# Kernel optimization log

Measured on AMD Instinct MI355X. Metric: run time of the kernel, lower is better.

Reference implementation:

```python
import jax, jax.numpy as jnp
import numpy as np

NUM_HEADS = 8
DIM_HEAD = 64
GROUPS = 32
EPS = 1e-5


def setup_inputs() -> dict:
    key = jax.random.key(0)
    k1, k2, k3 = jax.random.split(key, 3)
    C = 512
    inner = NUM_HEADS * DIM_HEAD  # 512
    x = jax.random.normal(k1, (8, C, 32, 32), dtype=jnp.float32)
    gamma = jnp.ones((C,), dtype=jnp.float32)
    beta = jnp.zeros((C,), dtype=jnp.float32)
    w_qkv = jax.random.normal(k2, (3 * inner, C), dtype=jnp.float32) * 0.02
    w_out = jax.random.normal(k3, (C, inner), dtype=jnp.float32) * 0.02
    return {"x": x, "gamma": gamma, "beta": beta, "w_qkv": w_qkv, "w_out": w_out}


def group_norm(x, gamma, beta):
    b, c, h, w = x.shape
    xg = x.reshape(b, GROUPS, c // GROUPS, h, w)
    mean = jnp.mean(xg, axis=(2, 3, 4), keepdims=True)
    var = jnp.var(xg, axis=(2, 3, 4), keepdims=True)
    xn = ((xg - mean) * jax.lax.rsqrt(var + EPS)).reshape(b, c, h, w)
    return xn * gamma[None, :, None, None] + beta[None, :, None, None]


def reference(x, gamma, beta, w_qkv, w_out):
    b, c, h, w = x.shape
    H, d = NUM_HEADS, DIM_HEAD
    inner = H * d
    scale = d ** (-0.5)
    residual = x
    xn = group_norm(x, gamma, beta)
    # 1x1 conv (no bias) == channel matmul
    qkv = jnp.einsum('bchw,oc->bohw', xn, w_qkv)  # [b, 3*inner, h, w]
    q, k, v = jnp.split(qkv, 3, axis=1)
    def to_heads(t):
        # b (H d) h w -> b H (h w) d
        return t.reshape(b, H, d, h * w).transpose(0, 1, 3, 2)
    q, k, v = to_heads(q), to_heads(k), to_heads(v)
    attn = jnp.einsum('bhid,bhjd->bhij', q, k) * scale  # [b,H,hw,hw]
    attn = jax.nn.softmax(attn, axis=-1)
    out = jnp.einsum('bhij,bhjd->bhid', attn, v)  # [b,H,hw,d]
    # b H (h w) d -> b (H d) h w
    out = out.transpose(0, 1, 3, 2).reshape(b, inner, h, w)
    out = jnp.einsum('bchw,oc->bohw', out, w_out)
    return out + residual
```

## Files before the change

### kernel.cpp

```cpp
#include <hip/hip_runtime.h>


typedef __attribute__((ext_vector_type(8))) short bf16x8;
typedef __attribute__((ext_vector_type(4))) float f32x4;

#define NB 8
#define NC 512
#define HW 1024
#define NHEAD 8
#define DHEAD 64
#define GROUPS 32
#define CPG 16
#define QKV_N 1536

#define GLL16(gaddr, ldsaddr)                                                  \
    __builtin_amdgcn_global_load_lds(                                          \
        (const __attribute__((address_space(1))) unsigned*)(gaddr),            \
        (__attribute__((address_space(3))) unsigned*)(ldsaddr), 16, 0, 0)

__device__ alignas(64) short g_xn[(size_t)8192 * 512];
__device__ alignas(64) short g_qkv[(size_t)8192 * 1536];
__device__ alignas(64) short g_vt[(size_t)64 * 64 * 1024];
__device__ alignas(64) short g_attno[(size_t)8192 * 512];
__device__ alignas(64) short g_wqkv[(size_t)1536 * 512];
__device__ alignas(64) short g_wout[(size_t)512 * 512];

__device__ __forceinline__ float b2f(short h) {
    union { unsigned u; float f; } v;
    v.u = ((unsigned)(unsigned short)h) << 16;
    return v.f;
}
__device__ __forceinline__ short f2b(float f) {
    union { float f; unsigned u; } v;
    v.f = f;
    unsigned r = v.u + 0x7fff + ((v.u >> 16) & 1);
    return (short)(r >> 16);
}

__global__ __launch_bounds__(256) void conv_weights(
    const float* __restrict__ wqkv, const float* __restrict__ wout) {
    int i = blockIdx.x * 256 + threadIdx.x;
    if (i < 1536 * 512) {
        float v = wqkv[i];
        if (i < 512 * 512) v *= 0.125f;
        g_wqkv[i] = f2b(v);
    }
    if (i < 512 * 512)  g_wout[i] = f2b(wout[i]);
}

__global__ __launch_bounds__(256) void gn_kernel(
    const float* __restrict__ x, const float* __restrict__ gamma,
    const float* __restrict__ beta) {
    int b = blockIdx.x >> 5, g = blockIdx.x & 31;
    int tid = threadIdx.x;
    __shared__ alignas(16) short tile[CPG][HW];
    __shared__ float red[2][4];
    __shared__ float sg[CPG], sb[CPG];
    if (tid < CPG) {
        int cg = g * CPG + tid;
        sg[tid] = gamma[cg];
        sb[tid] = beta[cg];
    }
    const float* xb = x + (size_t)b * NC * HW + (size_t)g * CPG * HW;
    float s1 = 0.f, s2 = 0.f;
    #pragma unroll
    for (int it = 0; it < 8; it++) {
        int idx = tid + it * 256;
        f32x4 v0 = *(const f32x4*)(xb + idx * 8);
        f32x4 v1 = *(const f32x4*)(xb + idx * 8 + 4);
        bf16x8 w;
        #pragma unroll
        for (int j = 0; j < 4; j++) {
            s1 += v0[j] + v1[j]; s2 += v0[j] * v0[j] + v1[j] * v1[j];
            w[j] = f2b(v0[j]); w[j + 4] = f2b(v1[j]);
        }
        *(bf16x8*)(&((short*)tile)[idx * 8]) = w;
    }
    #pragma unroll
    for (int off = 32; off; off >>= 1) { s1 += __shfl_xor(s1, off); s2 += __shfl_xor(s2, off); }
    int wid = tid >> 6;
    if ((tid & 63) == 0) { red[0][wid] = s1; red[1][wid] = s2; }
    __syncthreads();
    float t1 = red[0][0] + red[0][1] + red[0][2] + red[0][3];
    float t2 = red[1][0] + red[1][1] + red[1][2] + red[1][3];
    float mean = t1 * (1.f / 16384.f);
    float var  = t2 * (1.f / 16384.f) - mean * mean;
    float inv  = rsqrtf(var + 1e-5f);
    #pragma unroll
    for (int p = 0; p < 4; p++) {
        int s = tid * 4 + p;
        bf16x8 pk0, pk1;
        #pragma unroll
        for (int cc = 0; cc < 8; cc++) {
            pk0[cc] = f2b((b2f(tile[cc][s])     - mean) * inv * sg[cc]     + sb[cc]);
            pk1[cc] = f2b((b2f(tile[cc + 8][s]) - mean) * inv * sg[cc + 8] + sb[cc + 8]);
        }
        size_t dst = ((size_t)(b * HW + s)) * NC + g * CPG;
        *(bf16x8*)(g_xn + dst)     = pk0;
        *(bf16x8*)(g_xn + dst + 8) = pk1;
    }
}

__global__ __launch_bounds__(256) void gemm_qkv() {
    const int K = NC;
    int tid = threadIdx.x, lane = tid & 63, wid = tid >> 6;
    int quad = lane >> 4, l15 = lane & 15;
    int row0 = blockIdx.x * 128;
    int col0 = blockIdx.y * 128;
    __shared__ alignas(16) short sa[128 * 32];
    __shared__ alignas(16) short sbuf[128 * 32];
    int srow = wid * 32 + (lane >> 2);
    int scol = (lane & 3) * 8;
    const short* ga = g_xn   + (size_t)(row0 + srow) * K + scol;
    const short* gb = g_wqkv + (size_t)(col0 + srow) * K + scol;
    short* la = sa   + wid * 1024;
    short* lb = sbuf + wid * 1024;
    int mw = (wid >> 1) * 64, nw = (wid & 1) * 64;
    f32x4 acc[4][4] = {};
    for (int k = 0; k < K; k += 32) {
        GLL16(ga + k, la);
        GLL16(ga + (size_t)16 * K + k, la + 512);
        GLL16(gb + k, lb);
        GLL16(gb + (size_t)16 * K + k, lb + 512);
        __syncthreads();
        bf16x8 af[4], bfv[4];
        #pragma unroll
        for (int m = 0; m < 4; m++) af[m]  = *(const bf16x8*)&sa[(mw + m * 16 + l15) * 32 + quad * 8];
        #pragma unroll
        for (int n = 0; n < 4; n++) bfv[n] = *(const bf16x8*)&sbuf[(nw + n * 16 + l15) * 32 + quad * 8];
        #pragma unroll
        for (int m = 0; m < 4; m++)
            #pragma unroll
            for (int n = 0; n < 4; n++)
                acc[m][n] = __builtin_amdgcn_mfma_f32_16x16x32_bf16(af[m], bfv[n], acc[m][n], 0, 0, 0);
        __syncthreads();
    }
    #pragma unroll
    for (int m = 0; m < 4; m++)
        #pragma unroll
        for (int n = 0; n < 4; n++)
            #pragma unroll
            for (int r = 0; r < 4; r++) {
                int row = row0 + mw + m * 16 + quad * 4 + r;
                int col = col0 + nw + n * 16 + l15;
                g_qkv[(size_t)row * QKV_N + col] = f2b(acc[m][n][r]);
            }
}

__global__ __launch_bounds__(256) void transpose_v() {
    int bh = blockIdx.x & 63, st = blockIdx.x >> 6;
    int b = bh >> 3, h = bh & 7;
    int tid = threadIdx.x;
    __shared__ alignas(16) short tile[64][72];
    int s0 = st * 64;
    #pragma unroll
    for (int cc = 0; cc < 2; cc++) {
        int idx = tid + cc * 256;
        int s = idx >> 3, dc = idx & 7;
        *(bf16x8*)&tile[s][dc * 8] =
            *(const bf16x8*)(g_qkv + ((size_t)(b * HW + s0 + s)) * QKV_N + 1024 + h * DHEAD + dc * 8);
    }
    __syncthreads();
    #pragma unroll
    for (int cc = 0; cc < 2; cc++) {
        int idx = tid + cc * 256;
        int d = idx & 63, sc = idx >> 6;
        bf16x8 o;
        #pragma unroll
        for (int j = 0; j < 8; j++) o[j] = tile[sc * 8 + j][d];
        *(bf16x8*)(g_vt + ((size_t)(bh * 64 + d)) * HW + s0 + sc * 8) = o;
    }
}

__global__ __launch_bounds__(256) void attn_kernel() {
    int qt = blockIdx.x & 7, h = (blockIdx.x >> 3) & 7, b = blockIdx.x >> 6;
    int bh = b * 8 + h;
    int tid = threadIdx.x, lane = tid & 63, wid = tid >> 6;
    int quad = lane >> 4, l15 = lane & 15;
    __shared__ alignas(16) short kt[2][64][72];
    __shared__ alignas(16) short vt[2][64][72];
    __shared__ alignas(16) short pt[4][32][72];
    int qrow0 = qt * 128 + wid * 32;

    bf16x8 aq[2][2];
    #pragma unroll
    for (int mi = 0; mi < 2; mi++) {
        const short* qb = g_qkv + ((size_t)(b * HW + qrow0 + mi * 16 + l15)) * QKV_N + h * DHEAD + quad * 8;
        aq[mi][0] = *(const bf16x8*)qb;
        aq[mi][1] = *(const bf16x8*)(qb + 32);
    }
    f32x4 acc_o[2][4] = {};
    float l_part[2][4] = {};

    auto stage = [&](int it, int bufi) {
        int t0 = it * 64;
        #pragma unroll
        for (int cc = 0; cc < 2; cc++) {
            int idx = tid + cc * 256;
            int r8 = idx >> 3, c8 = idx & 7;
            *(bf16x8*)&kt[bufi][r8][c8 * 8] =
                *(const bf16x8*)(g_qkv + ((size_t)(b * HW + t0 + r8)) * QKV_N + 512 + h * DHEAD + c8 * 8);
            *(bf16x8*)&vt[bufi][r8][c8 * 8] =
                *(const bf16x8*)(g_vt + ((size_t)(bh * 64 + r8)) * HW + t0 + c8 * 8);
        }
    };

    stage(0, 0);
    __syncthreads();
    for (int it = 0; it < 16; it++) {
        int cur = it & 1;
        if (it < 15) stage(it + 1, cur ^ 1);
        f32x4 sv[2][4];
        #pragma unroll
        for (int sub = 0; sub < 4; sub++) {
            bf16x8 b0 = *(const bf16x8*)&kt[cur][sub * 16 + l15][quad * 8];
            bf16x8 b1 = *(const bf16x8*)&kt[cur][sub * 16 + l15][32 + quad * 8];
            #pragma unroll
            for (int mi = 0; mi < 2; mi++) {
                f32x4 z = {};
                z = __builtin_amdgcn_mfma_f32_16x16x32_bf16(aq[mi][0], b0, z, 0, 0, 0);
                z = __builtin_amdgcn_mfma_f32_16x16x32_bf16(aq[mi][1], b1, z, 0, 0, 0);
                sv[mi][sub] = z;
            }
        }
        #pragma unroll
        for (int mi = 0; mi < 2; mi++)
            #pragma unroll
            for (int sub = 0; sub < 4; sub++)
                #pragma unroll
                for (int r = 0; r < 4; r++) {
                    float e = __expf(sv[mi][sub][r]);
                    l_part[mi][r] += e;
                    pt[wid][mi * 16 + quad * 4 + r][sub * 16 + l15] = f2b(e);
                }
        bf16x8 ap[2][2];
        #pragma unroll
        for (int mi = 0; mi < 2; mi++) {
            ap[mi][0] = *(const bf16x8*)&pt[wid][mi * 16 + l15][quad * 8];
            ap[mi][1] = *(const bf16x8*)&pt[wid][mi * 16 + l15][32 + quad * 8];
        }
        #pragma unroll
        for (int nd = 0; nd < 4; nd++) {
            bf16x8 bv0 = *(const bf16x8*)&vt[cur][nd * 16 + l15][quad * 8];
            bf16x8 bv1 = *(const bf16x8*)&vt[cur][nd * 16 + l15][32 + quad * 8];
            #pragma unroll
            for (int mi = 0; mi < 2; mi++) {
                acc_o[mi][nd] = __builtin_amdgcn_mfma_f32_16x16x32_bf16(ap[mi][0], bv0, acc_o[mi][nd], 0, 0, 0);
                acc_o[mi][nd] = __builtin_amdgcn_mfma_f32_16x16x32_bf16(ap[mi][1], bv1, acc_o[mi][nd], 0, 0, 0);
            }
        }
        __syncthreads();
    }
    #pragma unroll
    for (int mi = 0; mi < 2; mi++)
        #pragma unroll
        for (int r = 0; r < 4; r++) {
            float l = l_part[mi][r];
            l += __shfl_xor(l, 1); l += __shfl_xor(l, 2);
            l += __shfl_xor(l, 4); l += __shfl_xor(l, 8);
            float invl = 1.f / l;
            size_t row = (size_t)(b * HW + qrow0 + mi * 16 + quad * 4 + r);
            #pragma unroll
            for (int nd = 0; nd < 4; nd++)
                g_attno[row * NC + h * DHEAD + nd * 16 + l15] = f2b(acc_o[mi][nd][r] * invl);
        }
}

__global__ __launch_bounds__(256) void gemm_out(
    const float* __restrict__ xres, float* __restrict__ out) {
    const int K = NC;
    int tid = threadIdx.x, lane = tid & 63, wid = tid >> 6;
    int quad = lane >> 4, l15 = lane & 15;
    int row0 = blockIdx.x * 128;
    int col0 = blockIdx.y * 128;
    __shared__ alignas(16) short sa[128 * 32];
    __shared__ alignas(16) short sbuf[128 * 32];
    int srow = wid * 32 + (lane >> 2);
    int scol = (lane & 3) * 8;
    const short* ga = g_wout  + (size_t)(row0 + srow) * K + scol;
    const short* gb = g_attno + (size_t)(col0 + srow) * K + scol;
    short* la = sa   + wid * 1024;
    short* lb = sbuf + wid * 1024;
    int mw = (wid >> 1) * 64, nw = (wid & 1) * 64;
    f32x4 acc[4][4] = {};
    for (int k = 0; k < K; k += 32) {
        GLL16(ga + k, la);
        GLL16(ga + (size_t)16 * K + k, la + 512);
        GLL16(gb + k, lb);
        GLL16(gb + (size_t)16 * K + k, lb + 512);
        __syncthreads();
        bf16x8 af[4], bfv[4];
        #pragma unroll
        for (int m = 0; m < 4; m++) af[m]  = *(const bf16x8*)&sa[(mw + m * 16 + l15) * 32 + quad * 8];
        #pragma unroll
        for (int n = 0; n < 4; n++) bfv[n] = *(const bf16x8*)&sbuf[(nw + n * 16 + l15) * 32 + quad * 8];
        #pragma unroll
        for (int m = 0; m < 4; m++)
            #pragma unroll
            for (int n = 0; n < 4; n++)
                acc[m][n] = __builtin_amdgcn_mfma_f32_16x16x32_bf16(af[m], bfv[n], acc[m][n], 0, 0, 0);
        __syncthreads();
    }
    #pragma unroll
    for (int m = 0; m < 4; m++)
        #pragma unroll
        for (int n = 0; n < 4; n++)
            #pragma unroll
            for (int r = 0; r < 4; r++) {
                int o  = row0 + mw + m * 16 + quad * 4 + r;
                int bs = col0 + nw + n * 16 + l15;
                size_t addr = (size_t)(bs >> 10) * ((size_t)NC * HW) + (size_t)o * HW + (bs & 1023);
                out[addr] = acc[m][n][r] + xres[addr];
            }
}

extern "C" void kernel_launch(void* const* d_in, const int* in_sizes, int n_in,
                              void* d_out, int out_size, void* d_ws, size_t ws_size,
                              hipStream_t stream) {
    const float* x     = (const float*)d_in[0];
    const float* gamma = (const float*)d_in[1];
    const float* beta  = (const float*)d_in[2];
    const float* wqkv  = (const float*)d_in[3];
    const float* wout  = (const float*)d_in[4];
    float* out = (float*)d_out;

    conv_weights<<<dim3(3072), dim3(256), 0, stream>>>(wqkv, wout);
    gn_kernel<<<dim3(NB * GROUPS), dim3(256), 0, stream>>>(x, gamma, beta);
    gemm_qkv<<<dim3(64, 12), dim3(256), 0, stream>>>();
    transpose_v<<<dim3(1024), dim3(256), 0, stream>>>();
    attn_kernel<<<dim3(512), dim3(256), 0, stream>>>();
    gemm_out<<<dim3(4, 64), dim3(256), 0, stream>>>(x, out);
}
```

Measured before the change: 163.0 us.

## Stage K/V tiles with global_load_lds into XOR-swizzled LDS, pack P stores

K and V tiles now go straight from global memory into LDS with the direct global_load_lds path instead of register round-trips, using an XOR swizzle on 16-byte chunks to avoid bank conflicts when the MFMA operands are read back. The P tile is stored transposed as packed bf16x4 words (round-to-nearest via bit add) and read back with scalar gathers. Block index mapping now puts bh in the low bits so neighbouring blocks share K/V. The risks are that nothing waits for the async LDS loads beyond the existing barrier, and that the 8 scalar LDS reads for P may cost more than the packed writes save.

```diff
diff --git a/kernel.cpp b/kernel.cpp
--- a/kernel.cpp
+++ b/kernel.cpp
@@ -2,6 +2,7 @@
 
 
 typedef __attribute__((ext_vector_type(8))) short bf16x8;
+typedef __attribute__((ext_vector_type(4))) short bf16x4;
 typedef __attribute__((ext_vector_type(4))) float f32x4;
 
 #define NB 8
@@ -173,13 +174,13 @@
 }
 
 __global__ __launch_bounds__(256) void attn_kernel() {
-    int qt = blockIdx.x & 7, h = (blockIdx.x >> 3) & 7, b = blockIdx.x >> 6;
-    int bh = b * 8 + h;
+    int bh = blockIdx.x & 63, qt = blockIdx.x >> 6;
+    int b = bh >> 3, h = bh & 7;
     int tid = threadIdx.x, lane = tid & 63, wid = tid >> 6;
     int quad = lane >> 4, l15 = lane & 15;
-    __shared__ alignas(16) short kt[2][64][72];
-    __shared__ alignas(16) short vt[2][64][72];
-    __shared__ alignas(16) short pt[4][32][72];
+    __shared__ alignas(16) short kt[2][64 * 64];
+    __shared__ alignas(16) short vt[2][64 * 64];
+    __shared__ alignas(16) short pt[4][64][36];
     int qrow0 = qt * 128 + wid * 32;
 
     bf16x8 aq[2][2];
@@ -192,16 +193,19 @@
     f32x4 acc_o[2][4] = {};
     float l_part[2][4] = {};
 
+    int r_lo = lane >> 3;
+    int s_log = (lane & 7) ^ r_lo;
+    int swz = l15 & 7;
+
     auto stage = [&](int it, int bufi) {
         int t0 = it * 64;
         #pragma unroll
-        for (int cc = 0; cc < 2; cc++) {
-            int idx = tid + cc * 256;
-            int r8 = idx >> 3, c8 = idx & 7;
-            *(bf16x8*)&kt[bufi][r8][c8 * 8] =
-                *(const bf16x8*)(g_qkv + ((size_t)(b * HW + t0 + r8)) * QKV_N + 512 + h * DHEAD + c8 * 8);
-            *(bf16x8*)&vt[bufi][r8][c8 * 8] =
-                *(const bf16x8*)(g_vt + ((size_t)(bh * 64 + r8)) * HW + t0 + c8 * 8);
+        for (int c = 0; c < 2; c++) {
+            int r = wid * 16 + c * 8 + r_lo;
+            GLL16(g_qkv + ((size_t)(b * HW + t0 + r)) * QKV_N + 512 + h * DHEAD + s_log * 8,
+                  &kt[bufi][(wid * 16 + c * 8) * 64]);
+            GLL16(g_vt + ((size_t)(bh * 64 + r)) * HW + t0 + s_log * 8,
+                  &vt[bufi][(wid * 16 + c * 8) * 64]);
         }
     };
 
@@ -213,8 +217,9 @@
         f32x4 sv[2][4];
         #pragma unroll
         for (int sub = 0; sub < 4; sub++) {
-            bf16x8 b0 = *(const bf16x8*)&kt[cur][sub * 16 + l15][quad * 8];
-            bf16x8 b1 = *(const bf16x8*)&kt[cur][sub * 16 + l15][32 + quad * 8];
+            int row = sub * 16 + l15;
+            bf16x8 b0 = *(const bf16x8*)&kt[cur][row * 64 + ((quad ^ swz) * 8)];
+            bf16x8 b1 = *(const bf16x8*)&kt[cur][row * 64 + (((4 + quad) ^ swz) * 8)];
             #pragma unroll
             for (int mi = 0; mi < 2; mi++) {
                 f32x4 z = {};
@@ -226,23 +231,35 @@
         #pragma unroll
         for (int mi = 0; mi < 2; mi++)
             #pragma unroll
-            for (int sub = 0; sub < 4; sub++)
+            for (int sub = 0; sub < 4; sub++) {
+                unsigned u[4];
                 #pragma unroll
                 for (int r = 0; r < 4; r++) {
                     float e = __expf(sv[mi][sub][r]);
                     l_part[mi][r] += e;
-                    pt[wid][mi * 16 + quad * 4 + r][sub * 16 + l15] = f2b(e);
+                    union { float f; unsigned b; } cv; cv.f = e;
+                    u[r] = cv.b + 0x8000u;
                 }
+                unsigned d0 = (u[0] >> 16) | (u[1] & 0xffff0000u);
+                unsigned d1 = (u[2] >> 16) | (u[3] & 0xffff0000u);
+                union { unsigned w[2]; bf16x4 s; } pk;
+                pk.w[0] = d0; pk.w[1] = d1;
+                *(bf16x4*)&pt[wid][sub * 16 + l15][mi * 16 + quad * 4] = pk.s;
+            }
+        asm volatile("" ::: "memory");
         bf16x8 ap[2][2];
         #pragma unroll
-        for (int mi = 0; mi < 2; mi++) {
-            ap[mi][0] = *(const bf16x8*)&pt[wid][mi * 16 + l15][quad * 8];
-            ap[mi][1] = *(const bf16x8*)&pt[wid][mi * 16 + l15][32 + quad * 8];
-        }
+        for (int mi = 0; mi < 2; mi++)
+            #pragma unroll
+            for (int j = 0; j < 8; j++) {
+                ap[mi][0][j] = pt[wid][quad * 8 + j][mi * 16 + l15];
+                ap[mi][1][j] = pt[wid][32 + quad * 8 + j][mi * 16 + l15];
+            }
         #pragma unroll
         for (int nd = 0; nd < 4; nd++) {
-            bf16x8 bv0 = *(const bf16x8*)&vt[cur][nd * 16 + l15][quad * 8];
-            bf16x8 bv1 = *(const bf16x8*)&vt[cur][nd * 16 + l15][32 + quad * 8];
+            int row = nd * 16 + l15;
+            bf16x8 bv0 = *(const bf16x8*)&vt[cur][row * 64 + ((quad ^ swz) * 8)];
+            bf16x8 bv1 = *(const bf16x8*)&vt[cur][row * 64 + (((4 + quad) ^ swz) * 8)];
             #pragma unroll
             for (int mi = 0; mi < 2; mi++) {
                 acc_o[mi][nd] = __builtin_amdgcn_mfma_f32_16x16x32_bf16(ap[mi][0], bv0, acc_o[mi][nd], 0, 0, 0);
```

Measured after the change: 157.1 us. -3.6%, faster.
